# Kernel tuning notes

Hardware: AMD Instinct MI355X
Metric: run time of the kernel (lower is better)

Reference implementation:

```python
import jax, jax.numpy as jnp
import numpy as np

N_NODES = 50000
N_EDGES = 400000
IN_F = 512
HID = 512      # 2 * out_features
OUT_F = 256
N_CELL = 1000
N_DIM = 128
N_SEL = 8192
N_C = 1024


def setup_inputs() -> dict:
    key = jax.random.key(0)
    ks = jax.random.split(key, 16)
    x = jax.random.normal(ks[0], (N_NODES, IN_F), dtype=jnp.float32)
    src = jax.random.randint(ks[1], (N_EDGES,), 0, N_NODES, dtype=jnp.int32)
    dst = jax.random.randint(ks[2], (N_EDGES,), 0, N_NODES, dtype=jnp.int32)
    x_indices = jax.random.randint(ks[3], (N_SEL,), 0, N_NODES, dtype=jnp.int32)
    c_indices = jax.random.randint(ks[4], (N_C,), 0, N_CELL, dtype=jnp.int32)
    s = lambda f: 1.0 / np.sqrt(f)
    W1 = jax.random.normal(ks[5], (IN_F, HID), dtype=jnp.float32) * s(IN_F)
    b1 = jnp.zeros((HID,), jnp.float32)
    W2 = jax.random.normal(ks[6], (HID, HID), dtype=jnp.float32) * s(HID)
    b2 = jnp.zeros((HID,), jnp.float32)
    W3 = jax.random.normal(ks[7], (HID, OUT_F), dtype=jnp.float32) * s(HID)
    b3 = jnp.zeros((OUT_F,), jnp.float32)
    Wp = jax.random.normal(ks[8], (OUT_F, N_DIM), dtype=jnp.float32) * s(OUT_F)
    bp = jnp.zeros((N_DIM,), jnp.float32)
    emb = jax.random.normal(ks[9], (N_CELL, N_DIM), dtype=jnp.float32)
    return {"x": x, "src": src, "dst": dst, "x_indices": x_indices,
            "c_indices": c_indices, "W1": W1, "b1": b1, "W2": W2, "b2": b2,
            "W3": W3, "b3": b3, "Wp": Wp, "bp": bp, "emb": emb}


def _degree_norms(src, dst, n):
    ones = jnp.ones(src.shape[0], jnp.float32)
    deg_out = jax.ops.segment_sum(ones, src, num_segments=n)
    deg_in = jax.ops.segment_sum(ones, dst, num_segments=n)
    ns = jnp.where(deg_out > 0, jax.lax.rsqrt(jnp.maximum(deg_out, 1.0)), 0.0)
    nd = jnp.where(deg_in > 0, jax.lax.rsqrt(jnp.maximum(deg_in, 1.0)), 0.0)
    return ns[:, None], nd[:, None]


def _gconv(h, src, dst, norm_src, norm_dst, W, b, n):
    # DGL GraphConv, norm='both': D_in^{-1/2} A D_out^{-1/2} H W + b
    msg = (h * norm_src)[src]                         # [E, F]
    agg = jax.ops.segment_sum(msg, dst, num_segments=n)
    return (agg * norm_dst) @ W + b


def reference(x, src, dst, x_indices, c_indices, W1, b1, W2, b2, W3, b3, Wp, bp, emb):
    n = x.shape[0]
    ns, nd = _degree_norms(src, dst, n)
    h = jax.nn.relu(_gconv(x, src, dst, ns, nd, W1, b1, n))
    h = jax.nn.relu(_gconv(h, src, dst, ns, nd, W2, b2, n))
    h = jax.nn.relu(_gconv(h, src, dst, ns, nd, W3, b3, n))
    enc = h[x_indices]                                # [N_SEL, OUT_F]
    proj = enc @ Wp + bp                              # Dropout in eval mode = identity
    e = emb[c_indices]                                # [N_C, N_DIM]
    return e @ proj.T                                 # [N_C, N_SEL]
```

## Files before the change

### kernel.cpp

```cpp
#include <hip/hip_runtime.h>

typedef unsigned int u32;
typedef unsigned short u16;

#define N_NODES 50000
#define N_EDGES 400000
#define IN_F 512
#define HID 512
#define OUT_F 256
#define N_CELL 1000
#define N_DIM 128
#define N_SEL 8192
#define N_C 1024
#define MPAD 50048

typedef __bf16 bf16x8 __attribute__((ext_vector_type(8)));
typedef float f32x4 __attribute__((ext_vector_type(4)));

__device__ __forceinline__ u16 f2bf(float f) {
    u32 u = __builtin_bit_cast(u32, f);
    u32 r = (u + 0x7fffu + ((u >> 16) & 1u)) >> 16;
    return (u16)r;
}
__device__ __forceinline__ float bf2f(u32 bits16) {
    return __builtin_bit_cast(float, bits16 << 16);
}

__device__ __forceinline__ void async_copy16(const u16* g, u16* l) {
    __builtin_amdgcn_global_load_lds(
        (const __attribute__((address_space(1))) void*)g,
        (__attribute__((address_space(3))) void*)l, 16, 0, 0);
}


__global__ void degrees_kernel(const int* __restrict__ src, const int* __restrict__ dst,
                               int* __restrict__ degO, int* __restrict__ degI) {
    int e = blockIdx.x * 256 + threadIdx.x;
    if (e < N_EDGES) {
        atomicAdd(&degO[src[e]], 1);
        atomicAdd(&degI[dst[e]], 1);
    }
}

__global__ void scan_kernel(const int* __restrict__ deg, int* __restrict__ offs) {
    __shared__ int sh[1024];
    const int t = threadIdx.x;
    const int chunk = (N_NODES + 1023) >> 10;
    const int start = t * chunk;
    const int end = min(start + chunk, N_NODES);
    int sum = 0;
    for (int i = start; i < end; ++i) sum += deg[i];
    sh[t] = sum;
    __syncthreads();
    for (int off = 1; off < 1024; off <<= 1) {
        int v = (t >= off) ? sh[t - off] : 0;
        __syncthreads();
        sh[t] += v;
        __syncthreads();
    }
    int run = sh[t] - sum;
    for (int i = start; i < end; ++i) { offs[i] = run; run += deg[i]; }
    if (end == N_NODES) offs[N_NODES] = run;
}

__global__ void fill_csr_kernel(const int* __restrict__ src, const int* __restrict__ dst,
                                int* __restrict__ cursor, const int* __restrict__ offs,
                                int* __restrict__ csr) {
    int e = blockIdx.x * 256 + threadIdx.x;
    if (e < N_EDGES) {
        int d = dst[e];
        int slot = atomicAdd(&cursor[d], 1);
        csr[offs[d] + slot] = src[e];
    }
}

__global__ void norms_kernel(const int* __restrict__ degO, const int* __restrict__ degI,
                             float* __restrict__ ns, float* __restrict__ nd) {
    int i = blockIdx.x * 256 + threadIdx.x;
    if (i < N_NODES) {
        ns[i] = degO[i] > 0 ? rsqrtf((float)degO[i]) : 0.f;
        nd[i] = degI[i] > 0 ? rsqrtf((float)degI[i]) : 0.f;
    }
}


__global__ void trans_bf16_kernel(const float* __restrict__ src, u16* __restrict__ dst,
                                  int K, int N) {
    int i = blockIdx.x * 256 + threadIdx.x;
    if (i >= K * N) return;
    int n = i / K, k = i % K;
    dst[i] = f2bf(src[k * N + n]);
}

__global__ void convert_x_kernel(const float* __restrict__ x, u16* __restrict__ xb) {
    int i = blockIdx.x * 256 + threadIdx.x;
    int base = i * 4;
    int m = base >> 9;
    ushort4 o;
    if (m < N_NODES) {
        float4 v = *(const float4*)(x + base);
        o.x = f2bf(v.x); o.y = f2bf(v.y); o.z = f2bf(v.z); o.w = f2bf(v.w);
    } else {
        o = make_ushort4(0, 0, 0, 0);
    }
    *(ushort4*)(xb + base) = o;
}

__global__ void gather_emb_kernel(const float* __restrict__ emb, const int* __restrict__ cidx,
                                  u16* __restrict__ eb) {
    int c = blockIdx.x, f = threadIdx.x;
    eb[c * N_DIM + f] = f2bf(emb[(size_t)cidx[c] * N_DIM + f]);
}

__global__ __launch_bounds__(256, 2) void gemm_bf16_nt(
    const u16* __restrict__ A, const u16* __restrict__ B,
    const int* __restrict__ aidx,
    u16* __restrict__ Cb, float* __restrict__ Cf,
    const float* __restrict__ scale, int nScale,
    const float* __restrict__ bias,
    int N, int K) {
    __shared__ __align__(16) u16 As[128 * 32];
    __shared__ __align__(16) u16 Bs[128 * 32];
    const int t = threadIdx.x;
    const int m0 = blockIdx.x * 128, n0 = blockIdx.y * 128;
    const int l = t & 63, w = t >> 6;
    const int wm = (w >> 1) << 6, wn = (w & 1) << 6;
    const int lr = l & 15, quad = l >> 4;

    const int lrow = l >> 2;
    const int kof = (l & 3) << 3;
    const int r0 = w, r1 = w + 4;
    int ar0 = m0 + r0 * 16 + lrow;
    int ar1 = m0 + r1 * 16 + lrow;
    if (aidx) { ar0 = aidx[ar0]; ar1 = aidx[ar1]; }
    const u16* gA0 = A + (size_t)ar0 * K + kof;
    const u16* gA1 = A + (size_t)ar1 * K + kof;
    const u16* gB0 = B + (size_t)(n0 + r0 * 16 + lrow) * K + kof;
    const u16* gB1 = B + (size_t)(n0 + r1 * 16 + lrow) * K + kof;
    u16* lA0 = As + r0 * 512;
    u16* lA1 = As + r1 * 512;
    u16* lB0 = Bs + r0 * 512;
    u16* lB1 = Bs + r1 * 512;

    f32x4 acc[4][4] = {};

    for (int ks = 0; ks < K; ks += 32) {
        async_copy16(gA0 + ks, lA0);
        async_copy16(gA1 + ks, lA1);
        async_copy16(gB0 + ks, lB0);
        async_copy16(gB1 + ks, lB1);
        __syncthreads();
        bf16x8 af[4], bg[4];
#pragma unroll
        for (int i = 0; i < 4; ++i)
            af[i] = *(const bf16x8*)&As[(wm + i * 16 + lr) * 32 + quad * 8];
#pragma unroll
        for (int j = 0; j < 4; ++j)
            bg[j] = *(const bf16x8*)&Bs[(wn + j * 16 + lr) * 32 + quad * 8];
#pragma unroll
        for (int i = 0; i < 4; ++i)
#pragma unroll
            for (int j = 0; j < 4; ++j)
                acc[i][j] = __builtin_amdgcn_mfma_f32_16x16x32_bf16(af[i], bg[j], acc[i][j], 0, 0, 0);
        __syncthreads();
    }

#pragma unroll
    for (int i = 0; i < 4; ++i) {
        int rbase = m0 + wm + i * 16 + quad * 4;
#pragma unroll
        for (int j = 0; j < 4; ++j) {
            int col = n0 + wn + j * 16 + lr;
            float bv = bias ? bias[col] : 0.f;
#pragma unroll
            for (int r = 0; r < 4; ++r) {
                int rg = rbase + r;
                float sc = scale ? (rg < nScale ? scale[rg] : 0.f) : 1.f;
                float v = acc[i][j][r] * sc + bv;
                if (Cb) Cb[(size_t)rg * N + col] = f2bf(v);
                else    Cf[(size_t)rg * N + col] = v;
            }
        }
    }
}

template <int W32>
struct AggVec;
template <> struct AggVec<4> { using T = uint4; };
template <> struct AggVec<2> { using T = uint2; };

template <int F>
__global__ __launch_bounds__(256) void aggregate_kernel(
    const u16* __restrict__ T, const int* __restrict__ csr,
    const int* __restrict__ offs, const float* __restrict__ nd,
    const float* __restrict__ bias, u16* __restrict__ H) {
    constexpr int W32 = F / 128;
    using VT = typename AggVec<W32>::T;
    const int t = threadIdx.x, w = t >> 6, l = t & 63;
    const int node = blockIdx.x * 4 + w;
    u32* __restrict__ Hrow = (u32*)H + (size_t)node * (F / 2) + l * W32;
    if (node >= N_NODES) {
        VT z = {};
        *(VT*)Hrow = z;
        return;
    }
    const int s0 = __builtin_amdgcn_readfirstlane(offs[node]);
    const int s1 = __builtin_amdgcn_readfirstlane(offs[node + 1]);
    const u32* __restrict__ Tb = (const u32*)T + l * W32;

    float acc[4][2 * W32];
#pragma unroll
    for (int c = 0; c < 4; ++c)
#pragma unroll
        for (int j = 0; j < 2 * W32; ++j) acc[c][j] = 0.f;

    int e = s0;
    for (; e + 4 <= s1; e += 4) {
        int si[4];
#pragma unroll
        for (int c = 0; c < 4; ++c) si[c] = csr[e + c];
        VT v[4];
#pragma unroll
        for (int c = 0; c < 4; ++c)
            v[c] = *(const VT*)(Tb + (size_t)si[c] * (F / 2));
#pragma unroll
        for (int c = 0; c < 4; ++c) {
            const u32* vv = (const u32*)&v[c];
#pragma unroll
            for (int j = 0; j < W32; ++j) {
                acc[c][2 * j] += bf2f(vv[j] & 0xffffu);
                acc[c][2 * j + 1] += bf2f(vv[j] >> 16);
            }
        }
    }
    for (; e < s1; ++e) {
        int s = csr[e];
        VT v = *(const VT*)(Tb + (size_t)s * (F / 2));
        const u32* vv = (const u32*)&v;
#pragma unroll
        for (int j = 0; j < W32; ++j) {
            acc[0][2 * j] += bf2f(vv[j] & 0xffffu);
            acc[0][2 * j + 1] += bf2f(vv[j] >> 16);
        }
    }

    const float ndv = nd[node];
    u32 ow[W32];
#pragma unroll
    for (int j = 0; j < W32; ++j) {
        float a0 = acc[0][2 * j] + acc[1][2 * j] + acc[2][2 * j] + acc[3][2 * j];
        float a1 = acc[0][2 * j + 1] + acc[1][2 * j + 1] + acc[2][2 * j + 1] + acc[3][2 * j + 1];
        float r0 = fmaxf(fmaf(a0, ndv, bias[l * 2 * W32 + 2 * j]), 0.f);
        float r1 = fmaxf(fmaf(a1, ndv, bias[l * 2 * W32 + 2 * j + 1]), 0.f);
        ow[j] = (u32)f2bf(r0) | ((u32)f2bf(r1) << 16);
    }
    VT o;
    u32* op = (u32*)&o;
#pragma unroll
    for (int j = 0; j < W32; ++j) op[j] = ow[j];
    *(VT*)Hrow = o;
}


extern "C" void kernel_launch(void* const* d_in, const int* in_sizes, int n_in,
                              void* d_out, int out_size, void* d_ws, size_t ws_size,
                              hipStream_t stream) {
    const float* x   = (const float*)d_in[0];
    const int*   src = (const int*)d_in[1];
    const int*   dst = (const int*)d_in[2];
    const int*   xidx= (const int*)d_in[3];
    const int*   cidx= (const int*)d_in[4];
    const float* W1  = (const float*)d_in[5];
    const float* b1  = (const float*)d_in[6];
    const float* W2  = (const float*)d_in[7];
    const float* b2  = (const float*)d_in[8];
    const float* W3  = (const float*)d_in[9];
    const float* b3  = (const float*)d_in[10];
    const float* Wp  = (const float*)d_in[11];
    const float* bp  = (const float*)d_in[12];
    const float* emb = (const float*)d_in[13];
    float* out = (float*)d_out;

    char* p = (char*)d_ws;
    auto alloc = [&](size_t bytes) {
        char* r = p;
        p += (bytes + 255) & ~(size_t)255;
        return r;
    };
    u16* T    = (u16*)alloc((size_t)MPAD * 512 * 2);
    u16* HX   = (u16*)alloc((size_t)MPAD * 512 * 2);
    u16* W1T  = (u16*)alloc((size_t)512 * 512 * 2);
    u16* W2T  = (u16*)alloc((size_t)512 * 512 * 2);
    u16* W3T  = (u16*)alloc((size_t)256 * 512 * 2);
    u16* WpT  = (u16*)alloc((size_t)128 * 256 * 2);
    u16* projb= (u16*)alloc((size_t)N_SEL * N_DIM * 2);
    u16* eb   = (u16*)alloc((size_t)N_C * N_DIM * 2);
    int* degO   = (int*)alloc(N_NODES * 4);
    int* degI   = (int*)alloc(N_NODES * 4);
    int* cursor = (int*)alloc(N_NODES * 4);
    int* offs   = (int*)alloc((N_NODES + 1) * 4);
    float* ns   = (float*)alloc(N_NODES * 4);
    float* nd   = (float*)alloc(N_NODES * 4);
    int* csr    = (int*)alloc(N_EDGES * 4);
    if ((size_t)(p - (char*)d_ws) > ws_size) return;

    hipMemsetAsync(degO, 0, (size_t)((char*)offs - (char*)degO), stream);
    degrees_kernel<<<(N_EDGES + 255) / 256, 256, 0, stream>>>(src, dst, degO, degI);
    scan_kernel<<<1, 1024, 0, stream>>>(degI, offs);
    fill_csr_kernel<<<(N_EDGES + 255) / 256, 256, 0, stream>>>(src, dst, cursor, offs, csr);
    norms_kernel<<<(N_NODES + 255) / 256, 256, 0, stream>>>(degO, degI, ns, nd);

    trans_bf16_kernel<<<(512 * 512) / 256, 256, 0, stream>>>(W1, W1T, 512, 512);
    trans_bf16_kernel<<<(512 * 512) / 256, 256, 0, stream>>>(W2, W2T, 512, 512);
    trans_bf16_kernel<<<(512 * 256) / 256, 256, 0, stream>>>(W3, W3T, 512, 256);
    trans_bf16_kernel<<<(256 * 128) / 256, 256, 0, stream>>>(Wp, WpT, 256, 128);
    convert_x_kernel<<<(MPAD * 512 / 4) / 256, 256, 0, stream>>>(x, HX);
    gather_emb_kernel<<<N_C, N_DIM, 0, stream>>>(emb, cidx, eb);

    gemm_bf16_nt<<<dim3(MPAD / 128, 512 / 128), 256, 0, stream>>>(
        HX, W1T, nullptr, T, nullptr, ns, N_NODES, nullptr, 512, 512);
    aggregate_kernel<512><<<MPAD / 4, 256, 0, stream>>>(T, csr, offs, nd, b1, HX);
    gemm_bf16_nt<<<dim3(MPAD / 128, 512 / 128), 256, 0, stream>>>(
        HX, W2T, nullptr, T, nullptr, ns, N_NODES, nullptr, 512, 512);
    aggregate_kernel<512><<<MPAD / 4, 256, 0, stream>>>(T, csr, offs, nd, b2, HX);
    gemm_bf16_nt<<<dim3(MPAD / 128, 256 / 128), 256, 0, stream>>>(
        HX, W3T, nullptr, T, nullptr, ns, N_NODES, nullptr, 256, 512);
    aggregate_kernel<256><<<MPAD / 4, 256, 0, stream>>>(T, csr, offs, nd, b3, HX);

    gemm_bf16_nt<<<dim3(N_SEL / 128, 1), 256, 0, stream>>>(
        HX, WpT, xidx, projb, nullptr, nullptr, 0, bp, N_DIM, 256);
    gemm_bf16_nt<<<dim3(N_C / 128, N_SEL / 128), 256, 0, stream>>>(
        eb, projb, nullptr, nullptr, out, nullptr, 0, nullptr, N_SEL, N_DIM);
}
```

Measured before the change: 680.1 us.

## Replace single-block degree scan with three-phase multi-block prefix scan

The CSR offset computation previously ran as one 1024-thread block where each thread serially summed and rewrote a contiguous chunk of degrees. It is now split into a per-block reduction, a scan of block sums, and a per-block scan that adds the block offset. This spreads the work across many CUs with coalesced accesses, at the cost of two extra kernel launches and small temporary buffers.

After: 612.7 us. 1.11x faster.

```diff
diff --git a/kernel.cpp b/kernel.cpp
--- a/kernel.cpp
+++ b/kernel.cpp
@@ -14,6 +14,9 @@
 #define N_C 1024
 #define MPAD 50048
 
+#define SCAN_B 256
+#define SCAN_NB ((N_NODES + SCAN_B - 1) / SCAN_B)
+
 typedef __bf16 bf16x8 __attribute__((ext_vector_type(8)));
 typedef float f32x4 __attribute__((ext_vector_type(4)));
 
@@ -42,25 +45,50 @@
     }
 }
 
-__global__ void scan_kernel(const int* __restrict__ deg, int* __restrict__ offs) {
-    __shared__ int sh[1024];
+__global__ void scan_blocksum_kernel(const int* __restrict__ deg, int* __restrict__ bsum) {
+    __shared__ int sh[SCAN_B];
+    int i = blockIdx.x * SCAN_B + threadIdx.x;
+    int v = (i < N_NODES) ? deg[i] : 0;
+    sh[threadIdx.x] = v;
+    __syncthreads();
+    for (int off = SCAN_B / 2; off > 0; off >>= 1) {
+        if (threadIdx.x < off) sh[threadIdx.x] += sh[threadIdx.x + off];
+        __syncthreads();
+    }
+    if (threadIdx.x == 0) bsum[blockIdx.x] = sh[0];
+}
+
+__global__ void scan_bsum_kernel(const int* __restrict__ bsum, int* __restrict__ boff) {
+    __shared__ int sh[SCAN_B];
     const int t = threadIdx.x;
-    const int chunk = (N_NODES + 1023) >> 10;
-    const int start = t * chunk;
-    const int end = min(start + chunk, N_NODES);
-    int sum = 0;
-    for (int i = start; i < end; ++i) sum += deg[i];
-    sh[t] = sum;
+    int v = (t < SCAN_NB) ? bsum[t] : 0;
+    sh[t] = v;
     __syncthreads();
-    for (int off = 1; off < 1024; off <<= 1) {
-        int v = (t >= off) ? sh[t - off] : 0;
-        __syncthreads();
-        sh[t] += v;
-        __syncthreads();
-    }
-    int run = sh[t] - sum;
-    for (int i = start; i < end; ++i) { offs[i] = run; run += deg[i]; }
-    if (end == N_NODES) offs[N_NODES] = run;
+    for (int off = 1; off < SCAN_B; off <<= 1) {
+        int u = (t >= off) ? sh[t - off] : 0;
+        __syncthreads();
+        sh[t] += u;
+        __syncthreads();
+    }
+    if (t < SCAN_NB) boff[t] = sh[t] - v;
+}
+
+__global__ void scan_final_kernel(const int* __restrict__ deg, const int* __restrict__ boff,
+                                  int* __restrict__ offs) {
+    __shared__ int sh[SCAN_B];
+    const int t = threadIdx.x;
+    int i = blockIdx.x * SCAN_B + t;
+    int v = (i < N_NODES) ? deg[i] : 0;
+    sh[t] = v;
+    __syncthreads();
+    for (int off = 1; off < SCAN_B; off <<= 1) {
+        int u = (t >= off) ? sh[t - off] : 0;
+        __syncthreads();
+        sh[t] += u;
+        __syncthreads();
+    }
+    if (i < N_NODES) offs[i] = boff[blockIdx.x] + sh[t] - v;
+    if (i == 0) offs[N_NODES] = N_EDGES;
 }
 
 __global__ void fill_csr_kernel(const int* __restrict__ src, const int* __restrict__ dst,
@@ -302,11 +330,15 @@
     float* ns   = (float*)alloc(N_NODES * 4);
     float* nd   = (float*)alloc(N_NODES * 4);
     int* csr    = (int*)alloc(N_EDGES * 4);
+    int* bsum   = (int*)alloc(SCAN_NB * 4);
+    int* boff   = (int*)alloc(SCAN_NB * 4);
     if ((size_t)(p - (char*)d_ws) > ws_size) return;
 
     hipMemsetAsync(degO, 0, (size_t)((char*)offs - (char*)degO), stream);
     degrees_kernel<<<(N_EDGES + 255) / 256, 256, 0, stream>>>(src, dst, degO, degI);
-    scan_kernel<<<1, 1024, 0, stream>>>(degI, offs);
+    scan_blocksum_kernel<<<SCAN_NB, SCAN_B, 0, stream>>>(degI, bsum);
+    scan_bsum_kernel<<<1, SCAN_B, 0, stream>>>(bsum, boff);
+    scan_final_kernel<<<SCAN_NB, SCAN_B, 0, stream>>>(degI, boff, offs);
     fill_csr_kernel<<<(N_EDGES + 255) / 256, 256, 0, stream>>>(src, dst, cursor, offs, csr);
     norms_kernel<<<(N_NODES + 255) / 256, 256, 0, stream>>>(degO, degI, ns, nd);
 
```
